# Kernel tuning notes

Hardware: AMD Instinct MI355X
Metric: run time of the kernel (lower is better)

Reference implementation:

```python
import jax, jax.numpy as jnp
import numpy as np

B, S, IN, D, HID, H, K, YD = 4, 2048, 64, 128, 400, 4, 20, 4
WHICH_OUT = 0
ALPHAS = jnp.array([0.05, 0.06, 0.08, 0.1, 0.12, 0.14, 0.15, 0.17, 0.19, 0.2,
                    0.21, 0.23, 0.25, 0.3, 0.35, 0.38, 0.4, 0.45], dtype=jnp.float32)  # 18 alphas


def _mlp(x, W1, b1, W2, b2, W3, b3, W4, b4):
    # FcModel encoder: in -> 400 -> 400 -> 400 -> out, ReLU hidden, linear head
    h = jax.nn.relu(x @ W1 + b1)
    h = jax.nn.relu(h @ W2 + b2)
    h = jax.nn.relu(h @ W3 + b3)
    return h @ W4 + b4


def _ln(x, g, b):
    mu = jnp.mean(x, axis=-1, keepdims=True)
    var = jnp.var(x, axis=-1, keepdims=True)
    return (x - mu) * jax.lax.rsqrt(var + 1e-5) * g + b


def setup_inputs() -> dict:
    key = jax.random.key(0)
    ks = jax.random.split(key, 16)
    w = lambda k, shape: 0.05 * jax.random.normal(k, shape, dtype=jnp.float32)
    return {
        'X_ctx_true': jax.random.normal(ks[0], (B, S, IN), dtype=jnp.float32),
        'X_ctx_sim':  jax.random.normal(ks[1], (B, S, IN), dtype=jnp.float32),
        'errors':     jax.random.normal(ks[2], (B, S, YD), dtype=jnp.float32),
        'y':          jax.random.normal(ks[3], (B, S, YD), dtype=jnp.float32),
        'y_pred':     jax.random.normal(ks[4], (B, S, YD), dtype=jnp.float32),
        'W1': w(ks[5], (IN, HID)),  'b1': jnp.zeros((HID,), jnp.float32),
        'W2': w(ks[6], (HID, HID)), 'b2': jnp.zeros((HID,), jnp.float32),
        'W3': w(ks[7], (HID, HID)), 'b3': jnp.zeros((HID,), jnp.float32),
        'W4': w(ks[8], (HID, D)),   'b4': jnp.zeros((D,), jnp.float32),
        'Wq': w(ks[9], (D, H * D)), 'bq': jnp.zeros((H * D,), jnp.float32),
        'Wk': w(ks[10], (D, H * D)), 'bk': jnp.zeros((H * D,), jnp.float32),
        'g_q': jnp.ones((D,), jnp.float32), 'beta_q': jnp.zeros((D,), jnp.float32),
        'g_k': jnp.ones((D,), jnp.float32), 'beta_k': jnp.zeros((D,), jnp.float32),
    }


def reference(X_ctx_true, X_ctx_sim, errors, y, y_pred,
              W1, b1, W2, b2, W3, b3, W4, b4,
              Wq, bq, Wk, bk, g_q, beta_q, g_k, beta_k):
    err_w = errors[..., WHICH_OUT]                      # [B,S]
    enc_true = _mlp(X_ctx_true, W1, b1, W2, b2, W3, b3, W4, b4)  # [B,S,D]
    enc_sim = _mlp(X_ctx_sim, W1, b1, W2, b2, W3, b3, W4, b4)    # [B,S,D]

    # Hopfield association: LayerNorm on state (query) and stored (key) patterns,
    # per-head projection to hidden_size=D, scaled dot product, diag mask, softmax.
    q = (_ln(enc_true, g_q, beta_q) @ Wq + bq).reshape(B, S, H, D)
    k = (_ln(enc_sim, g_k, beta_k) @ Wk + bk).reshape(B, S, H, D)
    scores = jnp.einsum('bshd,bmhd->bhsm', q, k) / jnp.sqrt(jnp.float32(D))
    diag = jnp.eye(S, dtype=bool)
    scores = jnp.where(diag[None, None], -jnp.inf, scores)
    assoc = jax.nn.softmax(scores, axis=-1)             # [B,H,S,M]

    # topk sampling of memory slots, gather corresponding errors
    _, idx = jax.lax.top_k(assoc, K)                    # [B,H,S,K]
    sel = err_w[jnp.arange(B)[:, None, None, None], idx]  # [B,H,S,K]

    # quantiles over samples for all alphas at once (torch.quantile = linear interp)
    betas = ALPHAS / 2.0
    q_low = jnp.quantile(sel, betas, axis=-1)           # [A,B,H,S]
    q_high = jnp.quantile(sel, 1.0 - ALPHAS + betas, axis=-1)  # [A,B,H,S]

    yp = y_pred[..., WHICH_OUT]                         # [B,S]
    y_low = q_low + yp[None, :, None, :]                # [A,B,H,S]
    y_high = q_high + yp[None, :, None, :]

    # mean-quantile MSE score, per head then averaged
    mean_err = jnp.concatenate([q_low, q_high], axis=0).mean(axis=0)  # [B,H,S]
    pred_adj = mean_err + yp[:, None, :]                # [B,H,S]
    y_true = y[..., WHICH_OUT]                          # [B,S]
    scores_per_head = jnp.mean((y_true[:, None, :] - pred_adj) ** 2, axis=(0, 2))  # [H]
    score = jnp.mean(scores_per_head)

    to_out = lambda a: jnp.transpose(a, (2, 1, 0, 3))[..., None]  # [A,B,H,S]->[H,B,A,S,1]
    return (score, y, y_pred, to_out(y_low), to_out(y_high),
            errors[..., WHICH_OUT:WHICH_OUT + 1], to_out(q_low), to_out(q_high))
```

## Files before the change

kernel.cpp:

```cpp
#include <hip/hip_runtime.h>
#include <hip/hip_bf16.h>
#include <math.h>


#define SS 2048
#define ROWS 16
#define AST 400

typedef short short8v __attribute__((ext_vector_type(8)));
typedef float float4v __attribute__((ext_vector_type(4)));
typedef float float2v __attribute__((ext_vector_type(2)));

__constant__ float c_alphas[18] = {0.05f,0.06f,0.08f,0.1f,0.12f,0.14f,0.15f,0.17f,
                                   0.19f,0.2f,0.21f,0.23f,0.25f,0.3f,0.35f,0.38f,0.4f,0.45f};

#define OFF_Y      1
#define OFF_YPRED  32769
#define OFF_YLOW   65537ll
#define OFF_YHIGH  655361ll
#define OFF_ERR    1245185ll
#define OFF_QLOW   1253377ll
#define OFF_QHIGH  1843201ll

__device__ inline short f2bf_s(float f) {
    __hip_bfloat16 h = __float2bfloat16(f);
    return __builtin_bit_cast(short, h);
}
__device__ inline unsigned mono(float f) {
    unsigned u = __builtin_bit_cast(unsigned, f);
    return (u & 0x80000000u) ? ~u : (u | 0x80000000u);
}
__device__ inline unsigned umin_(unsigned a, unsigned b) { return a < b ? a : b; }
__device__ inline unsigned umax_(unsigned a, unsigned b) { return a > b ? a : b; }


template<int IN_W, int WST, int AS>
__device__ __forceinline__ void layer_acc2(
    const float* __restrict__ W, const float* __restrict__ act,
    const int c0, float (&acc)[ROWS][2])
{
    #pragma unroll
    for (int r = 0; r < ROWS; ++r) { acc[r][0] = 0.f; acc[r][1] = 0.f; }
    #pragma unroll 2
    for (int i4 = 0; i4 < IN_W/4; ++i4) {
        float2 wv[4];
        #pragma unroll
        for (int jj = 0; jj < 4; ++jj)
            wv[jj] = *(const float2*)(W + (i4*4 + jj)*WST + c0);
        #pragma unroll
        for (int r = 0; r < ROWS; ++r) {
            const float4v xv = *(const float4v*)(act + r*AS + i4*4);
            #pragma unroll
            for (int jj = 0; jj < 4; ++jj) {
                acc[r][0] = fmaf(xv[jj], wv[jj].x, acc[r][0]);
                acc[r][1] = fmaf(xv[jj], wv[jj].y, acc[r][1]);
            }
        }
    }
}

template<int IN_W, int WST, int AS>
__device__ __forceinline__ void layer_acc1(
    const float* __restrict__ W, const float* __restrict__ act,
    const int jm, float (&acc)[ROWS][2])
{
    #pragma unroll
    for (int r = 0; r < ROWS; ++r) acc[r][0] = 0.f;
    #pragma unroll 2
    for (int i4 = 0; i4 < IN_W/4; ++i4) {
        float wv[4];
        #pragma unroll
        for (int jj = 0; jj < 4; ++jj)
            wv[jj] = W[(i4*4 + jj)*WST + jm];
        #pragma unroll
        for (int r = 0; r < ROWS; ++r) {
            const float4v xv = *(const float4v*)(act + r*AS + i4*4);
            #pragma unroll
            for (int jj = 0; jj < 4; ++jj)
                acc[r][0] = fmaf(xv[jj], wv[jj], acc[r][0]);
        }
    }
}

__device__ __forceinline__ void store2(
    const float* __restrict__ b, float* __restrict__ act,
    const int c0, const float (&acc)[ROWS][2])
{
    const float2 bb = *(const float2*)(b + c0);
    #pragma unroll
    for (int r = 0; r < ROWS; ++r) {
        float2 v;
        v.x = fmaxf(acc[r][0] + bb.x, 0.f);
        v.y = fmaxf(acc[r][1] + bb.y, 0.f);
        *(float2*)(&act[r*AST + c0]) = v;
    }
}

__device__ __forceinline__ void store1(
    const float* __restrict__ b, float* __restrict__ act,
    const int jm, const bool real, const float (&acc)[ROWS][2])
{
    if (real) {
        const float bv = b[jm];
        #pragma unroll
        for (int r = 0; r < ROWS; ++r)
            act[r*AST + jm] = fmaxf(acc[r][0] + bv, 0.f);
    }
}

__global__ __launch_bounds__(256, 4) void k_mlp(
    const float* __restrict__ Xt, const float* __restrict__ Xs,
    const float* __restrict__ W1, const float* __restrict__ b1,
    const float* __restrict__ W2, const float* __restrict__ b2,
    const float* __restrict__ W3, const float* __restrict__ b3,
    const float* __restrict__ W4, const float* __restrict__ b4,
    const float* __restrict__ Wq, const float* __restrict__ bq,
    const float* __restrict__ Wk, const float* __restrict__ bk,
    const float* __restrict__ g_q, const float* __restrict__ beta_q,
    const float* __restrict__ g_k, const float* __restrict__ beta_k,
    float* __restrict__ qf, float* __restrict__ kf,
    __hip_bfloat16* __restrict__ khi)
{
    __shared__ float act[ROWS*AST];

    const int tid  = threadIdx.x;
    const int t    = tid & 63;
    const int w    = tid >> 6;
    const int bi   = blockIdx.x;
    const int half = bi >> 9;
    const int rbase = (bi & 511) * ROWS;
    const float* X = half ? Xs : Xt;

    const int sl  = (w + bi) & 3;
    const int c0  = sl*128 + 2*t;
    const int jm  = (t < 16) ? (384 + t) : 399;
    const bool s3 = (sl == 3);

    #pragma unroll
    for (int u = 0; u < (ROWS*64)/256; ++u) {
        const int e = u*256 + tid;
        act[(e >> 6)*AST + (e & 63)] = X[(size_t)rbase*64 + e];
    }
    __syncthreads();

    float acc[ROWS][2];

    if (s3) layer_acc1<64,400,AST>(W1, act, jm, acc);
    else    layer_acc2<64,400,AST>(W1, act, c0, acc);
    __syncthreads();
    if (s3) store1(b1, act, jm, t < 16, acc);
    else    store2(b1, act, c0, acc);
    __syncthreads();

    if (s3) layer_acc1<400,400,AST>(W2, act, jm, acc);
    else    layer_acc2<400,400,AST>(W2, act, c0, acc);
    __syncthreads();
    if (s3) store1(b2, act, jm, t < 16, acc);
    else    store2(b2, act, c0, acc);
    __syncthreads();

    if (s3) layer_acc1<400,400,AST>(W3, act, jm, acc);
    else    layer_acc2<400,400,AST>(W3, act, c0, acc);
    __syncthreads();
    if (s3) store1(b3, act, jm, t < 16, acc);
    else    store2(b3, act, c0, acc);
    __syncthreads();

    float2v a4[4];
    #pragma unroll
    for (int rr = 0; rr < 4; ++rr) a4[rr] = (float2v){0.f, 0.f};
    #pragma unroll 2
    for (int i4 = 0; i4 < 100; ++i4) {
        float wv0[4], wv1[4];
        #pragma unroll
        for (int jj = 0; jj < 4; ++jj) {
            wv0[jj] = W4[(i4*4 + jj)*128 + t];
            wv1[jj] = W4[(i4*4 + jj)*128 + 64 + t];
        }
        #pragma unroll
        for (int rr = 0; rr < 4; ++rr) {
            const float4v xv = *(const float4v*)(act + (w*4 + rr)*AST + i4*4);
            #pragma unroll
            for (int jj = 0; jj < 4; ++jj) {
                a4[rr][0] = fmaf(xv[jj], wv0[jj], a4[rr][0]);
                a4[rr][1] = fmaf(xv[jj], wv1[jj], a4[rr][1]);
            }
        }
    }
    {
        const float b40 = b4[t], b41 = b4[64 + t];
        #pragma unroll
        for (int rr = 0; rr < 4; ++rr) { a4[rr][0] += b40; a4[rr][1] += b41; }
    }
    __syncthreads();

    {
        const float* g  = half ? g_k : g_q;
        const float* be = half ? beta_k : beta_q;
        const float gl0 = g[t],  gl1 = g[64 + t];
        const float bl0 = be[t], bl1 = be[64 + t];
        #pragma unroll
        for (int rr = 0; rr < 4; ++rr) {
            float s = a4[rr][0] + a4[rr][1];
            #pragma unroll
            for (int o = 32; o > 0; o >>= 1) s += __shfl_xor(s, o);
            const float mu = s * (1.f/128.f);
            const float d0 = a4[rr][0] - mu, d1 = a4[rr][1] - mu;
            float vs = d0*d0 + d1*d1;
            #pragma unroll
            for (int o = 32; o > 0; o >>= 1) vs += __shfl_xor(vs, o);
            const float rstd = rsqrtf(vs * (1.f/128.f) + 1e-5f);
            act[(w*4 + rr)*128 + t]      = d0*rstd*gl0 + bl0;
            act[(w*4 + rr)*128 + 64 + t] = d1*rstd*gl1 + bl1;
        }
    }
    __syncthreads();

    {
        const float* Wp = half ? Wk : Wq;
        const float* bp = half ? bk : bq;
        float* of = half ? kf : qf;

        float accp[ROWS][2];
        layer_acc2<128,512,128>(Wp, act, c0, accp);

        const float2 bpp = *(const float2*)(bp + c0);
        const int hh = c0 >> 7;
        const int d0 = c0 & 127;
        const int ks = d0 >> 5, qd = (d0 & 31) >> 3, jj0 = d0 & 7;
        #pragma unroll
        for (int r = 0; r < ROWS; ++r) {
            const int gidx = rbase + r;
            const int bB = gidx >> 11, s = gidx & 2047;
            const int T = s >> 4, m16s = s & 15;
            const float v0 = accp[r][0] + bpp.x;
            const float v1 = accp[r][1] + bpp.y;
            const size_t dst = ((size_t)(bB*4 + hh)*2048 + s)*128 + d0;
            *(float2*)(of + dst) = make_float2(v0, v1);
            if (half) {
                const size_t so = (size_t)(bB*4 + hh)*262144
                                + (size_t)T*2048 + ks*512 + qd*128 + m16s*8 + jj0;
                const unsigned pk = (unsigned)(unsigned short)f2bf_s(v0)
                                  | ((unsigned)(unsigned short)f2bf_s(v1) << 16);
                *reinterpret_cast<unsigned*>(khi + so) = pk;
            }
        }
    }
}

__global__ __launch_bounds__(256, 4) void k_scan(
    const float* __restrict__ qf, const __hip_bfloat16* __restrict__ khi,
    unsigned* __restrict__ wsk)
{
    __shared__ unsigned kd[64*97];

    const int tid   = threadIdx.x;
    const int stile = blockIdx.x;
    const int hb    = blockIdx.y;
    const int mq    = blockIdx.z;

    const int lane = tid & 63;
    const int w    = tid >> 6;
    const int m16  = lane & 15;
    const int quad = lane >> 4;

    const size_t slab = (size_t)hb * 2048;
    const __hip_bfloat16* slabp = khi + (size_t)hb * 262144;

    const int sg_my = stile*64 + w*16 + m16;

    short8v bq_[4];
    {
        const float* qp = qf + (slab + sg_my)*128 + quad*8;
        #pragma unroll
        for (int ks = 0; ks < 4; ++ks) {
            const float4 x0 = *(const float4*)(qp + ks*32);
            const float4 x1 = *(const float4*)(qp + ks*32 + 4);
            short8v tt;
            tt[0]=f2bf_s(x0.x); tt[1]=f2bf_s(x0.y); tt[2]=f2bf_s(x0.z); tt[3]=f2bf_s(x0.w);
            tt[4]=f2bf_s(x1.x); tt[5]=f2bf_s(x1.y); tt[6]=f2bf_s(x1.z); tt[7]=f2bf_s(x1.w);
            bq_[ks] = tt;
        }
    }

    unsigned KA[12], KB[12];
    #pragma unroll
    for (int n = 0; n < 12; ++n) { KA[n] = 0u; KB[n] = 0u; }

    #pragma unroll 1
    for (int cti = 0; cti < 32; ++cti) {
        const int T = mq*32 + cti;
        const __hip_bfloat16* kp = slabp + (size_t)T*2048 + lane*8;
        float4v acc = (float4v){0.f,0.f,0.f,0.f};
        #pragma unroll
        for (int ks = 0; ks < 4; ++ks) {
            const short8v ka = *(const short8v*)(kp + ks*512);
            acc = __builtin_amdgcn_mfma_f32_16x16x32_bf16(ka, bq_[ks], acc, 0, 0, 0);
        }
        const int cb = T*16 + quad*4;
        #pragma unroll
        for (int ph = 0; ph < 2; ++ph) {
            {
                const int m = cb + ph;
                unsigned key = (mono(acc[ph]) & 0xFFFFF800u) | (unsigned)m;
                key = (m == sg_my) ? 0u : key;
                KA[0] = umax_(KA[0], key);
                #pragma unroll
                for (int i = 0; i < 11; ++i) {
                    const unsigned a = KA[i], c = KA[i+1];
                    KA[i]   = umin_(a, c);
                    KA[i+1] = umax_(a, c);
                }
            }
            {
                const int m = cb + 2 + ph;
                unsigned key = (mono(acc[2+ph]) & 0xFFFFF800u) | (unsigned)m;
                key = (m == sg_my) ? 0u : key;
                KB[0] = umax_(KB[0], key);
                #pragma unroll
                for (int i = 0; i < 11; ++i) {
                    const unsigned a = KB[i], c = KB[i+1];
                    KB[i]   = umin_(a, c);
                    KB[i+1] = umax_(a, c);
                }
            }
        }
    }

    const int rr = w*16 + m16;
    #pragma unroll
    for (int n = 0; n < 12; ++n) {
        kd[rr*97 + (quad*2 + 0)*12 + n] = KA[11 - n];
        kd[rr*97 + (quad*2 + 1)*12 + n] = KB[11 - n];
    }
    __syncthreads();

    if (quad == 0) {
        const unsigned* R = &kd[rr*97];
        int q0=0,q1=0,q2=0,q3=0,q4=0,q5=0,q6=0,q7=0;
        const size_t base = (size_t)hb*2048 + stile*64 + rr;
        #pragma unroll 1
        for (int n = 0; n < 24; ++n) {
            const unsigned h0 = (q0<12)?R[  0+q0]:0u;
            const unsigned h1 = (q1<12)?R[ 12+q1]:0u;
            const unsigned h2 = (q2<12)?R[ 24+q2]:0u;
            const unsigned h3 = (q3<12)?R[ 36+q3]:0u;
            const unsigned h4 = (q4<12)?R[ 48+q4]:0u;
            const unsigned h5 = (q5<12)?R[ 60+q5]:0u;
            const unsigned h6 = (q6<12)?R[ 72+q6]:0u;
            const unsigned h7 = (q7<12)?R[ 84+q7]:0u;
            unsigned bv = h0; int bs = 0;
            if (h1 > bv) { bv = h1; bs = 1; }
            if (h2 > bv) { bv = h2; bs = 2; }
            if (h3 > bv) { bv = h3; bs = 3; }
            if (h4 > bv) { bv = h4; bs = 4; }
            if (h5 > bv) { bv = h5; bs = 5; }
            if (h6 > bv) { bv = h6; bs = 6; }
            if (h7 > bv) { bv = h7; bs = 7; }
            q0 += (bs==0); q1 += (bs==1); q2 += (bs==2); q3 += (bs==3);
            q4 += (bs==4); q5 += (bs==5); q6 += (bs==6); q7 += (bs==7);
            wsk[(size_t)(mq*24 + n)*32768 + base] = bv;
        }
    }
}

__global__ __launch_bounds__(256, 2) void k_select(
    const float* __restrict__ qf, const float* __restrict__ kf,
    const unsigned* __restrict__ wsk,
    const float* __restrict__ errors, const float* __restrict__ y,
    const float* __restrict__ y_pred,
    float* __restrict__ out, float* __restrict__ hacc)
{
    __shared__ unsigned kd[64*4*25];
    __shared__ unsigned short cb[64*33];
    __shared__ float es[64*33];
    __shared__ float ebuf[64*21];

    const int tid   = threadIdx.x;
    const int stile = blockIdx.x;
    const int hb    = blockIdx.y;
    const int b     = hb >> 2;
    const int h     = hb & 3;

    const int lane = tid & 63;
    const int w    = tid >> 6;
    const int m16  = lane & 15;
    const int quad = lane >> 4;
    const int rr   = w*16 + m16;
    const int sg   = stile*64 + rr;

    const size_t base = (size_t)hb*2048 + sg;
    #pragma unroll 1
    for (int n = 0; n < 24; ++n)
        kd[(rr*4 + quad)*25 + n] = wsk[(size_t)(quad*24 + n)*32768 + base];
    __syncthreads();

    if (quad == 0) {
        const unsigned* L0 = &kd[(rr*4 + 0)*25];
        const unsigned* L1 = &kd[(rr*4 + 1)*25];
        const unsigned* L2 = &kd[(rr*4 + 2)*25];
        const unsigned* L3 = &kd[(rr*4 + 3)*25];
        int p0 = 0, p1 = 0, p2 = 0, p3 = 0;
        #pragma unroll 1
        for (int n = 0; n < 32; ++n) {
            const unsigned h0 = (p0 < 24) ? L0[p0] : 0u;
            const unsigned h1 = (p1 < 24) ? L1[p1] : 0u;
            const unsigned h2 = (p2 < 24) ? L2[p2] : 0u;
            const unsigned h3 = (p3 < 24) ? L3[p3] : 0u;
            unsigned bv = h0; int bs = 0;
            if (h1 > bv) { bv = h1; bs = 1; }
            if (h2 > bv) { bv = h2; bs = 2; }
            if (h3 > bv) { bv = h3; bs = 3; }
            if (bs == 0) ++p0; else if (bs == 1) ++p1; else if (bs == 2) ++p2; else ++p3;
            cb[rr*33 + n] = (unsigned short)(bv & 0x7FFu);
        }
    }
    __syncthreads();

    const size_t slab = (size_t)hb * 2048;
    const float* qrow_p = qf + (slab + sg)*128;
    float4 qseg[8];
    #pragma unroll
    for (int u = 0; u < 8; ++u)
        qseg[u] = *(const float4*)(qrow_p + quad*4 + u*16);
    const float* kslab = kf + slab*128;
    #pragma unroll 1
    for (int n = 0; n < 32; ++n) {
        const int col = cb[rr*33 + n];
        const float* kc = kslab + (size_t)col*128 + quad*4;
        float2v s01 = (float2v){0.f, 0.f}, s23 = (float2v){0.f, 0.f};
        #pragma unroll
        for (int u = 0; u < 8; ++u) {
            const float4 kv = *(const float4*)(kc + u*16);
            s01 = __builtin_elementwise_fma((float2v){qseg[u].x, qseg[u].y},
                                            (float2v){kv.x, kv.y}, s01);
            s23 = __builtin_elementwise_fma((float2v){qseg[u].z, qseg[u].w},
                                            (float2v){kv.z, kv.w}, s23);
        }
        float v = (s01[0] + s01[1]) + (s23[0] + s23[1]);
        v += __shfl_xor(v, 16);
        v += __shfl_xor(v, 32);
        if (quad == 0) es[rr*33 + n] = v;
    }

    float sq = 0.f;
    if (quad == 0) {
        float rv[32]; int cvv[32];
        #pragma unroll
        for (int j = 0; j < 32; ++j) {
            rv[j]  = es[rr*33 + j];
            cvv[j] = (int)cb[rr*33 + j];
        }
        int bcs[20];
        #pragma unroll
        for (int k = 0; k < 20; ++k) {
            float best = -INFINITY; int bc = 4096, bj = 0;
            #pragma unroll
            for (int j = 0; j < 32; ++j) {
                const bool tk = (rv[j] > best) || (rv[j] == best && cvv[j] < bc);
                best = tk ? rv[j]  : best;
                bc   = tk ? cvv[j] : bc;
                bj   = tk ? j      : bj;
            }
            #pragma unroll
            for (int j = 0; j < 32; ++j)
                rv[j] = (j == bj) ? -INFINITY : rv[j];
            bcs[k] = bc;
        }
        float* e = &ebuf[rr*21];
        #pragma unroll
        for (int k = 0; k < 20; ++k)
            e[k] = errors[((size_t)(b*SS + bcs[k]))*4];
        #pragma unroll 1
        for (int a = 1; a < 20; ++a) {
            const float v = e[a];
            int n = a;
            while (n > 0 && e[n-1] > v) { e[n] = e[n-1]; --n; }
            e[n] = v;
        }
        const float yp = y_pred[((size_t)(b*SS + sg))*4];
        const float yt = y[((size_t)(b*SS + sg))*4];
        float msum = 0.f;
        const size_t obase = ((size_t)(h*4 + b)*18)*2048 + sg;
        #pragma unroll 1
        for (int a = 0; a < 18; ++a) {
            const float alpha = c_alphas[a];
            const float beta  = 0.5f*alpha;
            const float pl = beta * 19.f;
            const int   il = (int)pl;
            const float fl = pl - (float)il;
            const float ql = e[il]*(1.f-fl) + e[il+1]*fl;
            const float qq = (1.f - alpha) + beta;
            const float ph = qq * 19.f;
            const int   ih = (int)ph;
            const float fh = ph - (float)ih;
            const float qh = e[ih]*(1.f-fh) + e[ih+1]*fh;
            msum += ql + qh;
            const size_t oidx = obase + (size_t)a*2048;
            out[OFF_YLOW  + oidx] = ql + yp;
            out[OFF_YHIGH + oidx] = qh + yp;
            out[OFF_QLOW  + oidx] = ql;
            out[OFF_QHIGH + oidx] = qh;
        }
        const float me = msum * (1.f/36.f);
        const float dd = yt - (me + yp);
        sq = dd*dd;
    }
    #pragma unroll
    for (int o = 32; o > 0; o >>= 1) sq += __shfl_xor(sq, o);
    if (lane == 0) atomicAdd(&hacc[h], sq);
}

__global__ void k_init(float* __restrict__ hacc) {
    if (threadIdx.x < 4) hacc[threadIdx.x] = 0.f;
}

__global__ __launch_bounds__(256) void k_finalize(
    const float* __restrict__ y, const float* __restrict__ y_pred,
    const float* __restrict__ errors, const float* __restrict__ hacc,
    float* __restrict__ out)
{
    const int i = blockIdx.x*256 + threadIdx.x;
    if (i == 0)
        out[0] = (hacc[0]+hacc[1]+hacc[2]+hacc[3]) * (1.f/32768.f);
    if (i < 32768)      out[OFF_Y + i] = y[i];
    else if (i < 65536) out[OFF_YPRED + (i - 32768)] = y_pred[i - 32768];
    else if (i < 73728) { const int j = i - 65536; out[OFF_ERR + j] = errors[(size_t)j*4]; }
}

extern "C" void kernel_launch(void* const* d_in, const int* in_sizes, int n_in,
                              void* d_out, int out_size, void* d_ws, size_t ws_size,
                              hipStream_t stream)
{
    const float* Xt     = (const float*)d_in[0];
    const float* Xs     = (const float*)d_in[1];
    const float* errors = (const float*)d_in[2];
    const float* y      = (const float*)d_in[3];
    const float* y_pred = (const float*)d_in[4];
    const float* W1 = (const float*)d_in[5];   const float* b1 = (const float*)d_in[6];
    const float* W2 = (const float*)d_in[7];   const float* b2 = (const float*)d_in[8];
    const float* W3 = (const float*)d_in[9];   const float* b3 = (const float*)d_in[10];
    const float* W4 = (const float*)d_in[11];  const float* b4 = (const float*)d_in[12];
    const float* Wq = (const float*)d_in[13];  const float* bq = (const float*)d_in[14];
    const float* Wk = (const float*)d_in[15];  const float* bk = (const float*)d_in[16];
    const float* g_q    = (const float*)d_in[17];
    const float* beta_q = (const float*)d_in[18];
    const float* g_k    = (const float*)d_in[19];
    const float* beta_k = (const float*)d_in[20];

    float* out  = (float*)d_out;
    char*  base = (char*)d_ws;
    const size_t SLAB = (size_t)16*2048*128;
    float* hacc = (float*)base;
    float* qf   = (float*)(base + 256);
    float* kf   = qf + SLAB;
    __hip_bfloat16* khi = (__hip_bfloat16*)(kf + SLAB);
    unsigned* wsk = (unsigned*)(khi + SLAB);

    k_init<<<1, 64, 0, stream>>>(hacc);
    k_mlp<<<1024, 256, 0, stream>>>(Xt, Xs, W1,b1,W2,b2,W3,b3,W4,b4,
                                    Wq,bq,Wk,bk,g_q,beta_q,g_k,beta_k,
                                    qf, kf, khi);
    k_scan<<<dim3(32,16,4), 256, 0, stream>>>(qf, khi, wsk);
    k_select<<<dim3(32,16), 256, 0, stream>>>(qf, kf, wsk, errors, y, y_pred, out, hacc);
    k_finalize<<<288, 256, 0, stream>>>(y, y_pred, errors, hacc, out);
}
```

Before: 629.7 us.

## Give each wave its own rows in MLP layers and drop block barriers

Result: no change. 632.3 us (+0.4%).

```diff
diff --git a/kernel.cpp b/kernel.cpp
--- a/kernel.cpp
+++ b/kernel.cpp
@@ -35,76 +35,58 @@
 
 
 template<int IN_W, int WST, int AS>
-__device__ __forceinline__ void layer_acc2(
+__device__ __forceinline__ void layer_acc8(
     const float* __restrict__ W, const float* __restrict__ act,
-    const int c0, float (&acc)[ROWS][2])
-{
-    #pragma unroll
-    for (int r = 0; r < ROWS; ++r) { acc[r][0] = 0.f; acc[r][1] = 0.f; }
+    const int r0, const int c8, float4v (&acc0)[4], float4v (&acc1)[4])
+{
+    #pragma unroll
+    for (int r = 0; r < 4; ++r) {
+        acc0[r] = (float4v){0.f, 0.f, 0.f, 0.f};
+        acc1[r] = (float4v){0.f, 0.f, 0.f, 0.f};
+    }
+
     #pragma unroll 2
     for (int i4 = 0; i4 < IN_W/4; ++i4) {
-        float2 wv[4];
-        #pragma unroll
-        for (int jj = 0; jj < 4; ++jj)
-            wv[jj] = *(const float2*)(W + (i4*4 + jj)*WST + c0);
-        #pragma unroll
-        for (int r = 0; r < ROWS; ++r) {
-            const float4v xv = *(const float4v*)(act + r*AS + i4*4);
+        float4v w0[4], w1[4];
+        #pragma unroll
+        for (int jj = 0; jj < 4; ++jj) {
+            w0[jj] = *(const float4v*)(W + (i4*4 + jj)*WST + c8);
+            w1[jj] = *(const float4v*)(W + (i4*4 + jj)*WST + c8 + 4);
+        }
+        #pragma unroll
+        for (int r = 0; r < 4; ++r) {
+            const float4v xv = *(const float4v*)(act + (r0 + r)*AS + i4*4);
             #pragma unroll
             for (int jj = 0; jj < 4; ++jj) {
-                acc[r][0] = fmaf(xv[jj], wv[jj].x, acc[r][0]);
-                acc[r][1] = fmaf(xv[jj], wv[jj].y, acc[r][1]);
-            }
-        }
-    }
-}
-
-template<int IN_W, int WST, int AS>
-__device__ __forceinline__ void layer_acc1(
-    const float* __restrict__ W, const float* __restrict__ act,
-    const int jm, float (&acc)[ROWS][2])
-{
-    #pragma unroll
-    for (int r = 0; r < ROWS; ++r) acc[r][0] = 0.f;
-    #pragma unroll 2
-    for (int i4 = 0; i4 < IN_W/4; ++i4) {
-        float wv[4];
-        #pragma unroll
-        for (int jj = 0; jj < 4; ++jj)
-            wv[jj] = W[(i4*4 + jj)*WST + jm];
-        #pragma unroll
-        for (int r = 0; r < ROWS; ++r) {
-            const float4v xv = *(const float4v*)(act + r*AS + i4*4);
-            #pragma unroll
-            for (int jj = 0; jj < 4; ++jj)
-                acc[r][0] = fmaf(xv[jj], wv[jj], acc[r][0]);
-        }
-    }
-}
-
-__device__ __forceinline__ void store2(
+                #pragma unroll
+                for (int e = 0; e < 4; ++e)
+                    acc0[r][e] = fmaf(xv[jj], w0[jj][e], acc0[r][e]);
+                #pragma unroll
+                for (int e = 0; e < 4; ++e)
+                    acc1[r][e] = fmaf(xv[jj], w1[jj][e], acc1[r][e]);
+            }
+        }
+    }
+}
+
+__device__ __forceinline__ void store8(
     const float* __restrict__ b, float* __restrict__ act,
-    const int c0, const float (&acc)[ROWS][2])
-{
-    const float2 bb = *(const float2*)(b + c0);
-    #pragma unroll
-    for (int r = 0; r < ROWS; ++r) {
-        float2 v;
-        v.x = fmaxf(acc[r][0] + bb.x, 0.f);
-        v.y = fmaxf(acc[r][1] + bb.y, 0.f);
-        *(float2*)(&act[r*AST + c0]) = v;
-    }
-}
-
-__device__ __forceinline__ void store1(
-    const float* __restrict__ b, float* __restrict__ act,
-    const int jm, const bool real, const float (&acc)[ROWS][2])
-{
-    if (real) {
-        const float bv = b[jm];
-        #pragma unroll
-        for (int r = 0; r < ROWS; ++r)
-            act[r*AST + jm] = fmaxf(acc[r][0] + bv, 0.f);
+    const int r0, const int c8, const bool on,
+    const float4v (&acc0)[4], const float4v (&acc1)[4])
+{
+    if (!on) return;
+    const float4v b0 = *(const float4v*)(b + c8);
+    const float4v b1 = *(const float4v*)(b + c8 + 4);
+    #pragma unroll
+    for (int r = 0; r < 4; ++r) {
+        float4v v0, v1;
+        #pragma unroll
+        for (int e = 0; e < 4; ++e) {
+            v0[e] = fmaxf(acc0[r][e] + b0[e], 0.f);
+            v1[e] = fmaxf(acc1[r][e] + b1[e], 0.f);
+        }
+        *(float4v*)(act + (r0 + r)*AST + c8)     = v0;
+        *(float4v*)(act + (r0 + r)*AST + c8 + 4) = v1;
     }
 }
 
@@ -122,6 +104,7 @@
     __hip_bfloat16* __restrict__ khi)
 {
     __shared__ float act[ROWS*AST];
+    __shared__ float act2[ROWS*128];
 
     const int tid  = threadIdx.x;
     const int t    = tid & 63;
@@ -131,10 +114,9 @@
     const int rbase = (bi & 511) * ROWS;
     const float* X = half ? Xs : Xt;
 
-    const int sl  = (w + bi) & 3;
-    const int c0  = sl*128 + 2*t;
-    const int jm  = (t < 16) ? (384 + t) : 399;
-    const bool s3 = (sl == 3);
+    const int r0  = w*4;
+    const bool on = (t < 50);
+    const int c8  = on ? 8*t : 392;
 
     #pragma unroll
     for (int u = 0; u < (ROWS*64)/256; ++u) {
@@ -143,28 +125,16 @@
     }
     __syncthreads();
 
-    float acc[ROWS][2];
-
-    if (s3) layer_acc1<64,400,AST>(W1, act, jm, acc);
-    else    layer_acc2<64,400,AST>(W1, act, c0, acc);
-    __syncthreads();
-    if (s3) store1(b1, act, jm, t < 16, acc);
-    else    store2(b1, act, c0, acc);
-    __syncthreads();
-
-    if (s3) layer_acc1<400,400,AST>(W2, act, jm, acc);
-    else    layer_acc2<400,400,AST>(W2, act, c0, acc);
-    __syncthreads();
-    if (s3) store1(b2, act, jm, t < 16, acc);
-    else    store2(b2, act, c0, acc);
-    __syncthreads();
-
-    if (s3) layer_acc1<400,400,AST>(W3, act, jm, acc);
-    else    layer_acc2<400,400,AST>(W3, act, c0, acc);
-    __syncthreads();
-    if (s3) store1(b3, act, jm, t < 16, acc);
-    else    store2(b3, act, c0, acc);
-    __syncthreads();
+    float4v acc0[4], acc1[4];
+
+    layer_acc8<64,400,AST>(W1, act, r0, c8, acc0, acc1);
+    store8(b1, act, r0, c8, on, acc0, acc1);
+
+    layer_acc8<400,400,AST>(W2, act, r0, c8, acc0, acc1);
+    store8(b2, act, r0, c8, on, acc0, acc1);
+
+    layer_acc8<400,400,AST>(W3, act, r0, c8, acc0, acc1);
+    store8(b3, act, r0, c8, on, acc0, acc1);
 
     float2v a4[4];
     #pragma unroll
@@ -179,7 +149,7 @@
         }
         #pragma unroll
         for (int rr = 0; rr < 4; ++rr) {
-            const float4v xv = *(const float4v*)(act + (w*4 + rr)*AST + i4*4);
+            const float4v xv = *(const float4v*)(act + (r0 + rr)*AST + i4*4);
             #pragma unroll
             for (int jj = 0; jj < 4; ++jj) {
                 a4[rr][0] = fmaf(xv[jj], wv0[jj], a4[rr][0]);
@@ -192,7 +162,6 @@
         #pragma unroll
         for (int rr = 0; rr < 4; ++rr) { a4[rr][0] += b40; a4[rr][1] += b41; }
     }
-    __syncthreads();
 
     {
         const float* g  = half ? g_k : g_q;
@@ -210,39 +179,48 @@
             #pragma unroll
             for (int o = 32; o > 0; o >>= 1) vs += __shfl_xor(vs, o);
             const float rstd = rsqrtf(vs * (1.f/128.f) + 1e-5f);
-            act[(w*4 + rr)*128 + t]      = d0*rstd*gl0 + bl0;
-            act[(w*4 + rr)*128 + 64 + t] = d1*rstd*gl1 + bl1;
-        }
-    }
-    __syncthreads();
+            act2[(r0 + rr)*128 + t]      = d0*rstd*gl0 + bl0;
+            act2[(r0 + rr)*128 + 64 + t] = d1*rstd*gl1 + bl1;
+        }
+    }
 
     {
         const float* Wp = half ? Wk : Wq;
         const float* bp = half ? bk : bq;
         float* of = half ? kf : qf;
 
-        float accp[ROWS][2];
-        layer_acc2<128,512,128>(Wp, act, c0, accp);
-
-        const float2 bpp = *(const float2*)(bp + c0);
-        const int hh = c0 >> 7;
-        const int d0 = c0 & 127;
-        const int ks = d0 >> 5, qd = (d0 & 31) >> 3, jj0 = d0 & 7;
-        #pragma unroll
-        for (int r = 0; r < ROWS; ++r) {
-            const int gidx = rbase + r;
+        float4v ap0[4], ap1[4];
+        layer_acc8<128,512,128>(Wp, act2, r0, 8*t, ap0, ap1);
+
+        const float4v bp0 = *(const float4v*)(bp + 8*t);
+        const float4v bp1 = *(const float4v*)(bp + 8*t + 4);
+        const int j0 = 8*t;
+        const int hh = j0 >> 7;
+        const int d0 = j0 & 127;
+        const int ks = d0 >> 5, qd = (d0 & 31) >> 3;
+        #pragma unroll
+        for (int r = 0; r < 4; ++r) {
+            const int gidx = rbase + r0 + r;
             const int bB = gidx >> 11, s = gidx & 2047;
             const int T = s >> 4, m16s = s & 15;
-            const float v0 = accp[r][0] + bpp.x;
-            const float v1 = accp[r][1] + bpp.y;
+            float4v v0, v1;
+            #pragma unroll
+            for (int e = 0; e < 4; ++e) {
+                v0[e] = ap0[r][e] + bp0[e];
+                v1[e] = ap1[r][e] + bp1[e];
+            }
             const size_t dst = ((size_t)(bB*4 + hh)*2048 + s)*128 + d0;
-            *(float2*)(of + dst) = make_float2(v0, v1);
+            *(float4v*)(of + dst)     = v0;
+            *(float4v*)(of + dst + 4) = v1;
             if (half) {
                 const size_t so = (size_t)(bB*4 + hh)*262144
-                                + (size_t)T*2048 + ks*512 + qd*128 + m16s*8 + jj0;
-                const unsigned pk = (unsigned)(unsigned short)f2bf_s(v0)
-                                  | ((unsigned)(unsigned short)f2bf_s(v1) << 16);
-                *reinterpret_cast<unsigned*>(khi + so) = pk;
+                                + (size_t)T*2048 + ks*512 + qd*128 + m16s*8;
+                short8v kv;
+                kv[0]=f2bf_s(v0[0]); kv[1]=f2bf_s(v0[1]);
+                kv[2]=f2bf_s(v0[2]); kv[3]=f2bf_s(v0[3]);
+                kv[4]=f2bf_s(v1[0]); kv[5]=f2bf_s(v1[1]);
+                kv[6]=f2bf_s(v1[2]); kv[7]=f2bf_s(v1[3]);
+                *(short8v*)(khi + so) = kv;
             }
         }
     }
```
